# Optimization experiments

Measured on AMD Instinct MI355X. Metric: run time of the kernel, lower is better.

Reference implementation:

```python
import jax, jax.numpy as jnp
import numpy as np

N_NODES = 50000
N_EDGES = 800000
N_GRAPHS = 64
HIDDEN = 64


def setup_inputs() -> dict:
    key = jax.random.key(0)
    ks = jax.random.split(key, 16)
    inp = {
        "x": jax.random.normal(ks[0], (N_NODES, 1), dtype=jnp.float32),
        "edge_attr": jax.random.normal(ks[1], (N_EDGES, 1), dtype=jnp.float32),
        "edge_index": jax.random.randint(ks[2], (2, N_EDGES), 0, N_NODES, dtype=jnp.int32),
        "batch": jnp.sort(jax.random.randint(ks[3], (N_NODES,), 0, N_GRAPHS, dtype=jnp.int32)),
        # node/edge encoders: Linear(1, H)
        "W_node": jax.random.normal(ks[4], (1, HIDDEN), dtype=jnp.float32) * 0.1,
        "b_node": jnp.zeros((HIDDEN,), dtype=jnp.float32),
        "W_edge": jax.random.normal(ks[5], (1, HIDDEN), dtype=jnp.float32) * 0.1,
        "b_edge": jnp.zeros((HIDDEN,), dtype=jnp.float32),
        # message MLP: Linear(2H, H) + ReLU
        "W_msg": jax.random.normal(ks[6], (2 * HIDDEN, HIDDEN), dtype=jnp.float32) * (1.0 / np.sqrt(2 * HIDDEN)),
        "b_msg": jnp.zeros((HIDDEN,), dtype=jnp.float32),
        # update MLP: Linear(H, H) + ReLU
        "W_upd": jax.random.normal(ks[7], (HIDDEN, HIDDEN), dtype=jnp.float32) * (1.0 / np.sqrt(HIDDEN)),
        "b_upd": jnp.zeros((HIDDEN,), dtype=jnp.float32),
        # output: Linear(H, 1)
        "W_out": jax.random.normal(ks[8], (HIDDEN, 1), dtype=jnp.float32) * (1.0 / np.sqrt(HIDDEN)),
        "b_out": jnp.zeros((1,), dtype=jnp.float32),
    }
    return inp


def reference(x, edge_attr, edge_index, batch,
              W_node, b_node, W_edge, b_edge,
              W_msg, b_msg, W_upd, b_upd, W_out, b_out):
    # encoders
    h = x @ W_node + b_node                       # [N, H]
    e = edge_attr @ W_edge + b_edge               # [E, H]

    src, dst = edge_index[0], edge_index[1]
    x_j = h[src]                                  # gather source node feats [E, H]
    m = jax.nn.relu(jnp.concatenate([x_j, e], axis=-1) @ W_msg + b_msg)  # [E, H]

    # scatter-add aggregate to target nodes
    aggr = jax.ops.segment_sum(m, dst, num_segments=N_NODES)             # [N, H]

    # update MLP (applied to every node)
    upd = jax.nn.relu(aggr @ W_upd + b_upd)       # [N, H]

    # global mean pool per graph
    sums = jax.ops.segment_sum(upd, batch, num_segments=N_GRAPHS)        # [G, H]
    counts = jax.ops.segment_sum(jnp.ones((upd.shape[0],), dtype=upd.dtype), batch, num_segments=N_GRAPHS)
    avg = sums / jnp.maximum(counts, 1.0)[:, None]                       # [G, H]

    out = (avg @ W_out + b_out).squeeze(-1)       # [G]
    return out
```

## Files before the change

kernel.cpp:

```cpp
#include <hip/hip_runtime.h>

#define N_NODES 50000
#define N_EDGES 800000
#define N_GRAPHS 64
#define H 64
#define BN 64
#define NB ((N_NODES + BN - 1) / BN)
#define CAP 1280
#define CHUNK 2048
#define EPT (CHUNK / 256)
#define NCHUNK ((N_EDGES + CHUNK - 1) / CHUNK)
#define RPT ((CAP + 255) / 256)

#define VALS_OFF  0
#define ABC_OFF   (NB * CAP * 2)
#define GSUM_OFF  (ABC_OFF + 3 * H)
#define GCNT_OFF  (GSUM_OFF + N_GRAPHS)
#define BCUR_OFF  (GCNT_OFF + N_GRAPHS)

__global__ __launch_bounds__(256) void k_prep(
    int* __restrict__ bcur, float* __restrict__ abc,
    float* __restrict__ gsum, float* __restrict__ gcnt,
    const float* __restrict__ Wn, const float* __restrict__ bn,
    const float* __restrict__ We, const float* __restrict__ be,
    const float* __restrict__ Wm, const float* __restrict__ bm)
{
    const int t = threadIdx.x;
    for (int i = t; i < NB; i += 256) bcur[i] = 0;
    if (t < N_GRAPHS) { gsum[t] = 0.f; gcnt[t] = 0.f; }
    if (t < H) {
        const int k = t;
        float a = 0.f, b = 0.f, c = 0.f;
        #pragma unroll
        for (int i = 0; i < H; ++i) {
            float wt = Wm[i * H + k];
            float wb = Wm[(H + i) * H + k];
            a = fmaf(Wn[i], wt, a);
            b = fmaf(We[i], wb, b);
            c = fmaf(bn[i], wt, c);
            c = fmaf(be[i], wb, c);
        }
        abc[k]         = a;
        abc[H + k]     = b;
        abc[2 * H + k] = c + bm[k];
    }
}

__global__ __launch_bounds__(256) void k_bin(
    const float* __restrict__ x, const float* __restrict__ ea,
    const int* __restrict__ ei, int* __restrict__ bcur,
    float2* __restrict__ vals)
{
    __shared__ int lh[NB], lbase[NB], lcur[NB];
    const int t = threadIdx.x;
    for (int b = t; b < NB; b += 256) { lh[b] = 0; lcur[b] = 0; }

    const int e0 = blockIdx.x * CHUNK;
    const int* __restrict__ src = ei;
    const int* __restrict__ dst = ei + N_EDGES;

    int   d[EPT];
    float xv[EPT], ev[EPT];
    bool  ok[EPT];
    #pragma unroll
    for (int k = 0; k < EPT; ++k) {
        const int e = e0 + t + k * 256;
        ok[k] = (e < N_EDGES);
        const int ee = ok[k] ? e : (N_EDGES - 1);
        const int s  = src[ee];
        d[k]  = dst[ee];
        ev[k] = ea[ee];
        xv[k] = x[s];
    }
    __syncthreads();

    #pragma unroll
    for (int k = 0; k < EPT; ++k)
        if (ok[k]) atomicAdd(&lh[d[k] >> 6], 1);
    __syncthreads();

    for (int b = t; b < NB; b += 256) {
        const int v = lh[b];
        if (v) lbase[b] = atomicAdd(&bcur[b], v);
    }
    __syncthreads();

    #pragma unroll
    for (int k = 0; k < EPT; ++k) {
        if (ok[k]) {
            const int b  = d[k] >> 6;
            const int lp = atomicAdd(&lcur[b], 1);
            const unsigned uy = (__float_as_uint(ev[k]) & 0xFFFFFFC0u) |
                                (unsigned)(d[k] & (BN - 1));
            vals[b * CAP + lbase[b] + lp] = make_float2(xv[k], __uint_as_float(uy));
        }
    }
}

__global__ __launch_bounds__(256) void k_fused(
    const float2* __restrict__ vals, const int* __restrict__ bcur,
    const float* __restrict__ abc, const float* __restrict__ Wu,
    const float* __restrict__ bu, const float* __restrict__ Wo,
    const int* __restrict__ batch,
    float* __restrict__ gsum, float* __restrict__ gcnt)
{
    __shared__ float2 stB[CAP];
    __shared__ int lh[BN], le[BN], lc[BN];
    __shared__ __align__(16) float sA[4][72];
    __shared__ float lsum[N_GRAPHS], lcnt[N_GRAPHS];

    const int t    = threadIdx.x;
    const int lane = t & 63;
    const int w    = t >> 6;
    const int b    = blockIdx.x;
    const int base = b * CAP;

    const float A   = abc[lane];
    const float B   = abc[H + lane];
    const float C   = abc[2 * H + lane];
    const float bul = bu[lane];
    const float wol = Wo[lane];
    float wr[64];
    #pragma unroll
    for (int i = 0; i < 64; ++i) wr[i] = Wu[i * H + lane];

    if (t < BN) lh[t] = 0;
    if (t < N_GRAPHS) { lsum[t] = 0.f; lcnt[t] = 0.f; }
    __syncthreads();

    int m = bcur[b];
    if (m > CAP) m = CAP;

    float2 r[RPT];
    #pragma unroll
    for (int k = 0; k < RPT; ++k) {
        const int i = t + k * 256;
        if (i < m) {
            r[k] = vals[base + i];
            atomicAdd(&lh[__float_as_uint(r[k].y) & (BN - 1)], 1);
        }
    }
    __syncthreads();

    if (t < BN) {
        const int v = lh[t];
        int incl = v;
        #pragma unroll
        for (int d = 1; d < BN; d <<= 1) {
            const int up = __shfl_up(incl, d);
            if (lane >= d) incl += up;
        }
        le[t] = incl - v;
        lc[t] = incl - v;
    }
    __syncthreads();

    #pragma unroll
    for (int k = 0; k < RPT; ++k) {
        const int i = t + k * 256;
        if (i < m) {
            const int rk = atomicAdd(&lc[__float_as_uint(r[k].y) & (BN - 1)], 1);
            stB[rk] = r[k];
        }
    }
    __syncthreads();

    #define MSG(q) fmaxf(fmaf((q).x, A, fmaf((q).y, B, C)), 0.f)
    for (int qn = 0; qn < BN / 4; ++qn) {
        const int ln   = w * (BN / 4) + qn;
        const int node = b * BN + ln;
        const int off  = le[ln];
        const int c    = lh[ln];

        float s0 = 0.f, s1 = 0.f, s2 = 0.f, s3 = 0.f;
        int j = 0;
        for (; j + 8 <= c; j += 8) {
            const float2 q0 = stB[off + j + 0], q1 = stB[off + j + 1];
            const float2 q2 = stB[off + j + 2], q3 = stB[off + j + 3];
            const float2 q4 = stB[off + j + 4], q5 = stB[off + j + 5];
            const float2 q6 = stB[off + j + 6], q7 = stB[off + j + 7];
            s0 += MSG(q0); s1 += MSG(q1); s2 += MSG(q2); s3 += MSG(q3);
            s0 += MSG(q4); s1 += MSG(q5); s2 += MSG(q6); s3 += MSG(q7);
        }
        for (; j < c; ++j) { const float2 q = stB[off + j]; s0 += MSG(q); }
        const float s = (s0 + s1) + (s2 + s3);

        sA[w][lane] = s;
        float t0 = 0.f, t1 = 0.f, t2 = 0.f, t3 = 0.f;
        #pragma unroll
        for (int i = 0; i < 64; i += 4) {
            const float4 av = *(const float4*)&sA[w][i];
            t0 = fmaf(av.x, wr[i + 0], t0);
            t1 = fmaf(av.y, wr[i + 1], t1);
            t2 = fmaf(av.z, wr[i + 2], t2);
            t3 = fmaf(av.w, wr[i + 3], t3);
        }
        const float tk = (t0 + t1) + (t2 + t3);
        float u = fmaxf(tk + bul, 0.f) * wol;
        #pragma unroll
        for (int off2 = 32; off2 > 0; off2 >>= 1)
            u += __shfl_xor(u, off2);
        if (lane == 0 && node < N_NODES) {
            const int g = batch[node];
            atomicAdd(&lsum[g], u);
            atomicAdd(&lcnt[g], 1.f);
        }
    }
    #undef MSG
    __syncthreads();
    if (t < N_GRAPHS && lcnt[t] != 0.f) {
        atomicAdd(&gsum[t], lsum[t]);
        atomicAdd(&gcnt[t], lcnt[t]);
    }
}

__global__ void k_final(const float* __restrict__ gsum,
                        const float* __restrict__ gcnt,
                        const float* __restrict__ bo,
                        float* __restrict__ out)
{
    const int g = threadIdx.x;
    if (g < N_GRAPHS)
        out[g] = gsum[g] / fmaxf(gcnt[g], 1.f) + bo[0];
}

extern "C" void kernel_launch(void* const* d_in, const int* in_sizes, int n_in,
                              void* d_out, int out_size, void* d_ws, size_t ws_size,
                              hipStream_t stream)
{
    const float* x      = (const float*)d_in[0];
    const float* ea     = (const float*)d_in[1];
    const int*   ei     = (const int*)  d_in[2];
    const int*   batch  = (const int*)  d_in[3];
    const float* Wn     = (const float*)d_in[4];
    const float* bn     = (const float*)d_in[5];
    const float* We     = (const float*)d_in[6];
    const float* be     = (const float*)d_in[7];
    const float* Wm     = (const float*)d_in[8];
    const float* bm     = (const float*)d_in[9];
    const float* Wu     = (const float*)d_in[10];
    const float* bu     = (const float*)d_in[11];
    const float* Wo     = (const float*)d_in[12];
    const float* bo     = (const float*)d_in[13];

    float*  ws   = (float*)d_ws;
    float2* vals = (float2*)(ws + VALS_OFF);
    float*  abc  = ws + ABC_OFF;
    float*  gsum = ws + GSUM_OFF;
    float*  gcnt = ws + GCNT_OFF;
    int*    bcur = (int*)(ws + BCUR_OFF);
    float*  out  = (float*)d_out;

    k_prep<<<1, 256, 0, stream>>>(bcur, abc, gsum, gcnt, Wn, bn, We, be, Wm, bm);
    k_bin<<<NCHUNK, 256, 0, stream>>>(x, ea, ei, bcur, vals);
    k_fused<<<NB, 256, 0, stream>>>(vals, bcur, abc, Wu, bu, Wo, batch, gsum, gcnt);
    k_final<<<1, 64, 0, stream>>>(gsum, gcnt, bo, out);
}
```

Baseline: 58.53 us.

## Fold prep and final kernels into neighbors, memset workspace, halve bin chunk

Removes the single-block prep kernel by zeroing counters with a memset and computing the folded encoder/message coefficients inside block 0 of the binning kernel. The final averaging kernel is replaced by a last-block-done pattern in the fused kernel, using an atomic counter and threadfence. Binning chunk size is halved so more blocks run, each with fewer edges. This cuts launch overhead and serialization between tiny kernels, at the cost of extra atomics on global counters and more binning blocks doing global bucket atomics.

Result: slower. 120.4 us (+105.6%).

```diff
diff --git a/kernel.cpp b/kernel.cpp
--- a/kernel.cpp
+++ b/kernel.cpp
@@ -7,49 +7,27 @@
 #define BN 64
 #define NB ((N_NODES + BN - 1) / BN)
 #define CAP 1280
-#define CHUNK 2048
+#define CHUNK 1024
 #define EPT (CHUNK / 256)
 #define NCHUNK ((N_EDGES + CHUNK - 1) / CHUNK)
 #define RPT ((CAP + 255) / 256)
 
 #define VALS_OFF  0
 #define ABC_OFF   (NB * CAP * 2)
-#define GSUM_OFF  (ABC_OFF + 3 * H)
+#define ZERO_OFF  (ABC_OFF + 3 * H)
+#define GSUM_OFF  (ZERO_OFF)
 #define GCNT_OFF  (GSUM_OFF + N_GRAPHS)
-#define BCUR_OFF  (GCNT_OFF + N_GRAPHS)
-
-__global__ __launch_bounds__(256) void k_prep(
-    int* __restrict__ bcur, float* __restrict__ abc,
-    float* __restrict__ gsum, float* __restrict__ gcnt,
+#define DONE_OFF  (GCNT_OFF + N_GRAPHS)
+#define BCUR_OFF  (DONE_OFF + 2)
+#define ZERO_BYTES ((2 * N_GRAPHS + 2 + NB) * 4)
+
+__global__ __launch_bounds__(256) void k_bin(
+    const float* __restrict__ x, const float* __restrict__ ea,
+    const int* __restrict__ ei, int* __restrict__ bcur,
+    float2* __restrict__ vals, float* __restrict__ abc,
     const float* __restrict__ Wn, const float* __restrict__ bn,
     const float* __restrict__ We, const float* __restrict__ be,
     const float* __restrict__ Wm, const float* __restrict__ bm)
-{
-    const int t = threadIdx.x;
-    for (int i = t; i < NB; i += 256) bcur[i] = 0;
-    if (t < N_GRAPHS) { gsum[t] = 0.f; gcnt[t] = 0.f; }
-    if (t < H) {
-        const int k = t;
-        float a = 0.f, b = 0.f, c = 0.f;
-        #pragma unroll
-        for (int i = 0; i < H; ++i) {
-            float wt = Wm[i * H + k];
-            float wb = Wm[(H + i) * H + k];
-            a = fmaf(Wn[i], wt, a);
-            b = fmaf(We[i], wb, b);
-            c = fmaf(bn[i], wt, c);
-            c = fmaf(be[i], wb, c);
-        }
-        abc[k]         = a;
-        abc[H + k]     = b;
-        abc[2 * H + k] = c + bm[k];
-    }
-}
-
-__global__ __launch_bounds__(256) void k_bin(
-    const float* __restrict__ x, const float* __restrict__ ea,
-    const int* __restrict__ ei, int* __restrict__ bcur,
-    float2* __restrict__ vals)
 {
     __shared__ int lh[NB], lbase[NB], lcur[NB];
     const int t = threadIdx.x;
@@ -95,19 +73,38 @@
             vals[b * CAP + lbase[b] + lp] = make_float2(xv[k], __uint_as_float(uy));
         }
     }
+
+    if (blockIdx.x == 0 && t < H) {
+        const int k = t;
+        float a = 0.f, b = 0.f, c = 0.f;
+        #pragma unroll
+        for (int i = 0; i < H; ++i) {
+            float wt = Wm[i * H + k];
+            float wb = Wm[(H + i) * H + k];
+            a = fmaf(Wn[i], wt, a);
+            b = fmaf(We[i], wb, b);
+            c = fmaf(bn[i], wt, c);
+            c = fmaf(be[i], wb, c);
+        }
+        abc[k]         = a;
+        abc[H + k]     = b;
+        abc[2 * H + k] = c + bm[k];
+    }
 }
 
 __global__ __launch_bounds__(256) void k_fused(
     const float2* __restrict__ vals, const int* __restrict__ bcur,
     const float* __restrict__ abc, const float* __restrict__ Wu,
     const float* __restrict__ bu, const float* __restrict__ Wo,
-    const int* __restrict__ batch,
-    float* __restrict__ gsum, float* __restrict__ gcnt)
+    const int* __restrict__ batch, const float* __restrict__ bo,
+    float* __restrict__ gsum, float* __restrict__ gcnt,
+    int* __restrict__ done, float* __restrict__ out)
 {
     __shared__ float2 stB[CAP];
     __shared__ int lh[BN], le[BN], lc[BN];
     __shared__ __align__(16) float sA[4][72];
     __shared__ float lsum[N_GRAPHS], lcnt[N_GRAPHS];
+    __shared__ int isLast;
 
     const int t    = threadIdx.x;
     const int lane = t & 63;
@@ -212,16 +209,16 @@
         atomicAdd(&gsum[t], lsum[t]);
         atomicAdd(&gcnt[t], lcnt[t]);
     }
-}
-
-__global__ void k_final(const float* __restrict__ gsum,
-                        const float* __restrict__ gcnt,
-                        const float* __restrict__ bo,
-                        float* __restrict__ out)
-{
-    const int g = threadIdx.x;
-    if (g < N_GRAPHS)
-        out[g] = gsum[g] / fmaxf(gcnt[g], 1.f) + bo[0];
+    __threadfence();
+    __syncthreads();
+    if (t == 0)
+        isLast = (atomicAdd(done, 1) == NB - 1);
+    __syncthreads();
+    if (isLast && t < N_GRAPHS) {
+        const float gs = atomicAdd(&gsum[t], 0.f);
+        const float gc = atomicAdd(&gcnt[t], 0.f);
+        out[t] = gs / fmaxf(gc, 1.f) + bo[0];
+    }
 }
 
 extern "C" void kernel_launch(void* const* d_in, const int* in_sizes, int n_in,
@@ -248,11 +245,13 @@
     float*  abc  = ws + ABC_OFF;
     float*  gsum = ws + GSUM_OFF;
     float*  gcnt = ws + GCNT_OFF;
+    int*    done = (int*)(ws + DONE_OFF);
     int*    bcur = (int*)(ws + BCUR_OFF);
     float*  out  = (float*)d_out;
 
-    k_prep<<<1, 256, 0, stream>>>(bcur, abc, gsum, gcnt, Wn, bn, We, be, Wm, bm);
-    k_bin<<<NCHUNK, 256, 0, stream>>>(x, ea, ei, bcur, vals);
-    k_fused<<<NB, 256, 0, stream>>>(vals, bcur, abc, Wu, bu, Wo, batch, gsum, gcnt);
-    k_final<<<1, 64, 0, stream>>>(gsum, gcnt, bo, out);
+    hipMemsetAsync(ws + ZERO_OFF, 0, ZERO_BYTES, stream);
+    k_bin<<<NCHUNK, 256, 0, stream>>>(x, ea, ei, bcur, vals, abc,
+                                      Wn, bn, We, be, Wm, bm);
+    k_fused<<<NB, 256, 0, stream>>>(vals, bcur, abc, Wu, bu, Wo, batch, bo,
+                                    gsum, gcnt, done, out);
 }
```
